# Optimization experiments

Hardware: AMD Instinct MI355X
Metric: run time of the kernel (lower is better)

## Reference

```python
import jax, jax.numpy as jnp
import numpy as np


def setup_inputs() -> dict:
    key = jax.random.key(0)
    k1, k2, k3 = jax.random.split(key, 3)
    B, S, E = 4, 8192, 1024
    x = jax.random.normal(k1, (B, S, E), dtype=jnp.float32)
    # torch nn.Linear weights have shape [out_features, in_features]
    W1 = jax.random.normal(k2, (3 * E, E), dtype=jnp.float32) * (1.0 / np.sqrt(E))
    W2 = jax.random.normal(k3, (E, E), dtype=jnp.float32) * (1.0 / np.sqrt(E))
    return {"x": x, "W1": W1, "W2": W2, "heads": 16}


def reference(x, W1, W2, heads):
    B, S, E = x.shape
    h = heads
    e = E // h
    # qkv projection: [B,S,3E] -> 'b s (n h e) -> n b h s e'
    qkv = (x @ W1.T).reshape(B, S, 3, h, e)
    qkv = jnp.transpose(qkv, (2, 0, 3, 1, 4))  # [3,B,h,S,e]
    q, k, v = qkv[0], qkv[1], qkv[2]
    # score: [B,h,e,e], softmax over last dim (c)
    score = jax.nn.softmax(jnp.einsum('bhnk,bhnc->bhkc', k / 4, v), axis=-1)
    # einsum 'bhnk,bhkc->bhnk': elementwise over k, sum over c
    attn = jax.nn.softmax(jnp.einsum('bhnk,bhkc->bhnk', q / 4, score), axis=-1)
    # 'b h s e -> b s (h e)' then linear_2
    out = jnp.transpose(attn, (0, 2, 1, 3)).reshape(B, S, E) @ W2.T
    return out
```

## Files before the change

kernel.cpp:

```cpp
#include <hip/hip_runtime.h>
#include <hip/hip_bf16.h>
#include <stdint.h>

static constexpr int MTOT = 32768;
static constexpr int KD   = 1024;
static constexpr int ND   = 1024;

static constexpr int BM = 256, BN = 256, BK = 64;
static constexpr int NT = KD / BK;
static constexpr int BUF_BYTES = 65536;
static constexpr int BOFF = 32768;
static constexpr int HALF = 16384;

typedef __bf16 bf16x8 __attribute__((ext_vector_type(8)));
typedef float  f32x4  __attribute__((ext_vector_type(4)));

__device__ __forceinline__ unsigned short f2bf_rne(float f) {
  union { float f; uint32_t u; } c; c.f = f;
  uint32_t u = c.u;
  return (unsigned short)((u + 0x7fffu + ((u >> 16) & 1u)) >> 16);
}

__global__ void cast_f32_to_bf16(const float* __restrict__ src,
                                 unsigned short* __restrict__ dst, int n4) {
  int idx = blockIdx.x * blockDim.x + threadIdx.x;
  int stride = gridDim.x * blockDim.x;
  for (int i = idx; i < n4; i += stride) {
    float4 v = reinterpret_cast<const float4*>(src)[i];
    ushort4 o;
    o.x = f2bf_rne(v.x); o.y = f2bf_rne(v.y);
    o.z = f2bf_rne(v.z); o.w = f2bf_rne(v.w);
    reinterpret_cast<ushort4*>(dst)[i] = o;
  }
}

__device__ __forceinline__ void gload_lds16(const void* g, void* lds) {
  __builtin_amdgcn_global_load_lds(
      (const __attribute__((address_space(1))) unsigned int*)g,
      (__attribute__((address_space(3))) unsigned int*)lds, 16, 0, 0);
}

template <int SOFTMAX>
__global__ __launch_bounds__(512, 2)
void gemm8(const unsigned short* __restrict__ A,
           const unsigned short* __restrict__ Bm,
           void* __restrict__ Cout) {
  extern __shared__ __align__(16) char ldsc[];

  const int tid  = threadIdx.x;
  const int lane = tid & 63;
  const int wid  = tid >> 6;
  const int wm = wid >> 2, wn = wid & 3;
  const int fr = lane & 15, fq = lane >> 4;
  const int bid  = blockIdx.x;
  const int brow = (bid >> 2) * BM;
  const int bcol = (bid & 3) * BN;

  const int srow  = tid >> 3;
  const int sslot = (tid & 7) ^ (srow & 7);
  const unsigned short* gA = A  + (size_t)(brow + srow) * KD + sslot * 8;
  const unsigned short* gB = Bm + (size_t)(bcol + srow) * KD + sslot * 8;
  const int wofs = wid << 10;

  f32x4  acc[8][4] = {};
  bf16x8 a0[4][2], a1[4][2], bb[2][2];

  auto STAGE = [&](const unsigned short* g, int h, int kt, int b, int opOff) {
    const unsigned short* gu = g + (size_t)(h * 128) * KD + kt * BK;
    char* du = ldsc + b * BUF_BYTES + opOff + h * HALF + wofs;
    gload_lds16(gu, du);
    gload_lds16(gu + (size_t)64 * KD, du + 8192);
  };

  auto rdA = [&](int b, bf16x8 (*dst)[2], int mBase) {
    const char* base = ldsc + b * BUF_BYTES + wm * HALF;
    #pragma unroll
    for (int mm = 0; mm < 4; ++mm) {
      const int r = (mBase + mm) * 16 + fr;
      #pragma unroll
      for (int ks = 0; ks < 2; ++ks)
        dst[mm][ks] = *(const bf16x8*)(base + (r << 7) +
                        ((ks * 64 + fq * 16) ^ ((r & 7) << 4)));
    }
  };
  auto rdB = [&](int b, int nBase) {
    const char* base = ldsc + b * BUF_BYTES + BOFF + (wn >> 1) * HALF;
    #pragma unroll
    for (int nn = 0; nn < 2; ++nn) {
      const int r = (wn & 1) * 64 + (nBase + nn) * 16 + fr;
      #pragma unroll
      for (int ks = 0; ks < 2; ++ks)
        bb[nn][ks] = *(const bf16x8*)(base + (r << 7) +
                       ((ks * 64 + fq * 16) ^ ((r & 7) << 4)));
    }
  };
  auto MFMA16 = [&](int mBase, int nBase, bf16x8 (*af)[2]) {
    #pragma unroll
    for (int mm = 0; mm < 4; ++mm)
      #pragma unroll
      for (int nn = 0; nn < 2; ++nn)
        #pragma unroll
        for (int ks = 0; ks < 2; ++ks)
          acc[mBase + mm][nBase + nn] = __builtin_amdgcn_mfma_f32_16x16x32_bf16(
              af[mm][ks], bb[nn][ks], acc[mBase + mm][nBase + nn], 0, 0, 0);
  };

  STAGE(gA, 0, 0, 0, 0);    STAGE(gA, 1, 0, 0, 0);
  STAGE(gB, 0, 0, 0, BOFF); STAGE(gB, 1, 0, 0, BOFF);
  STAGE(gA, 0, 1, 1, 0);    STAGE(gA, 1, 1, 1, 0);
  asm volatile("s_waitcnt vmcnt(4)" ::: "memory");
  __builtin_amdgcn_s_barrier();

  for (int T = 0; T < NT; ++T) {
    const int cur = T & 1, nxt = cur ^ 1;
    const int tp1 = (T + 1 < NT) ? T + 1 : NT - 1;
    const int tp2 = (T + 2 < NT) ? T + 2 : NT - 1;

    rdA(cur, a0, 0); rdB(cur, 0);
    STAGE(gB, 0, tp1, nxt, BOFF);
    __builtin_amdgcn_s_barrier();
    asm volatile("s_waitcnt lgkmcnt(0)" ::: "memory");
    __builtin_amdgcn_s_setprio(1);
    MFMA16(0, 0, a0);
    __builtin_amdgcn_s_setprio(0);
    __builtin_amdgcn_s_barrier();

    rdA(cur, a1, 4);
    STAGE(gB, 1, tp1, nxt, BOFF);
    __builtin_amdgcn_s_barrier();
    asm volatile("s_waitcnt lgkmcnt(0)" ::: "memory");
    __builtin_amdgcn_s_setprio(1);
    MFMA16(4, 0, a1);
    __builtin_amdgcn_s_setprio(0);
    __builtin_amdgcn_s_barrier();

    rdB(cur, 2);
    STAGE(gA, 0, tp2, cur, 0);
    __builtin_amdgcn_s_barrier();
    asm volatile("s_waitcnt lgkmcnt(0)" ::: "memory");
    __builtin_amdgcn_s_setprio(1);
    MFMA16(4, 2, a1);
    __builtin_amdgcn_s_setprio(0);
    __builtin_amdgcn_s_barrier();

    STAGE(gA, 1, tp2, cur, 0);
    asm volatile("s_waitcnt vmcnt(4)" ::: "memory");
    __builtin_amdgcn_s_barrier();
    __builtin_amdgcn_s_setprio(1);
    MFMA16(0, 2, a0);
    __builtin_amdgcn_s_setprio(0);
    __builtin_amdgcn_s_barrier();
  }

  if constexpr (SOFTMAX) {
    unsigned short* attn = reinterpret_cast<unsigned short*>(Cout);
    constexpr float CEXP = 0.25f * 1.44269504088896340736f;
    #pragma unroll
    for (int m = 0; m < 8; ++m) {
      const int row = brow + wm * 128 + m * 16 + fq * 4;
      #pragma unroll
      for (int j = 0; j < 4; ++j) {
        float v0 = acc[m][0][j], v1 = acc[m][1][j];
        float v2 = acc[m][2][j], v3 = acc[m][3][j];
        float mx = fmaxf(fmaxf(v0, v1), fmaxf(v2, v3));
        #pragma unroll
        for (int s = 1; s < 16; s <<= 1) mx = fmaxf(mx, __shfl_xor(mx, s, 64));
        float p0 = exp2f((v0 - mx) * CEXP);
        float p1 = exp2f((v1 - mx) * CEXP);
        float p2 = exp2f((v2 - mx) * CEXP);
        float p3 = exp2f((v3 - mx) * CEXP);
        float sm = p0 + p1 + p2 + p3;
        #pragma unroll
        for (int s = 1; s < 16; s <<= 1) sm += __shfl_xor(sm, s, 64);
        const float inv = 1.0f / sm;
        unsigned short* dst =
            attn + (size_t)(row + j) * ND + (bcol + wn * 64 + fr);
        dst[0]  = f2bf_rne(p0 * inv);
        dst[16] = f2bf_rne(p1 * inv);
        dst[32] = f2bf_rne(p2 * inv);
        dst[48] = f2bf_rne(p3 * inv);
      }
    }
  } else {
    float* Cf = reinterpret_cast<float*>(Cout);
    #pragma unroll
    for (int m = 0; m < 8; ++m) {
      const int row = brow + wm * 128 + m * 16 + fq * 4;
      #pragma unroll
      for (int n = 0; n < 4; ++n) {
        const int col = bcol + wn * 64 + n * 16 + fr;
        #pragma unroll
        for (int j = 0; j < 4; ++j)
          Cf[(size_t)(row + j) * ND + col] = acc[m][n][j];
      }
    }
  }
}

extern "C" void kernel_launch(void* const* d_in, const int* in_sizes, int n_in,
                              void* d_out, int out_size, void* d_ws, size_t ws_size,
                              hipStream_t stream) {
  const float* x  = (const float*)d_in[0];
  const float* W1 = (const float*)d_in[1];
  const float* W2 = (const float*)d_in[2];
  float* out = (float*)d_out;

  char* ws = (char*)d_ws;
  unsigned short* xb   = (unsigned short*)(ws);
  unsigned short* w1b  = (unsigned short*)(ws + (size_t)67108864);
  unsigned short* w2b  = (unsigned short*)(ws + (size_t)69206016);
  unsigned short* attn = (unsigned short*)(ws + (size_t)71303168);

  hipFuncSetAttribute(reinterpret_cast<const void*>(gemm8<1>),
                      hipFuncAttributeMaxDynamicSharedMemorySize, 131072);
  hipFuncSetAttribute(reinterpret_cast<const void*>(gemm8<0>),
                      hipFuncAttributeMaxDynamicSharedMemorySize, 131072);

  cast_f32_to_bf16<<<2048, 256, 0, stream>>>(x,  xb,  MTOT * KD / 4);
  cast_f32_to_bf16<<<512,  256, 0, stream>>>(W1, w1b, KD * KD / 4);
  cast_f32_to_bf16<<<512,  256, 0, stream>>>(W2, w2b, KD * KD / 4);

  const int nblk = (MTOT / BM) * (ND / BN);
  gemm8<1><<<nblk, 512, 131072, stream>>>(xb, w1b, (void*)attn);
  gemm8<0><<<nblk, 512, 131072, stream>>>(attn, w2b, (void*)out);
}
```

Measured before the change: 205.8 us.

## Prefetch next tile's B fragments during last MFMA phase and remap block order

Splits the B fragment registers into two sets. The first B fragments of the next K tile are now read from LDS during the final MFMA phase of the current iteration, so the first phase no longer waits on that read. It also remaps block indices so that consecutive workgroups spread across row tiles in groups of eight, which changes L2 reuse of the A and B operands. The cost is more live VGPRs, which risks spilling under a launch bound of 512 threads with 2 blocks per CU.

```diff
diff --git a/kernel.cpp b/kernel.cpp
--- a/kernel.cpp
+++ b/kernel.cpp
@@ -52,7 +52,9 @@
   const int wid  = tid >> 6;
   const int wm = wid >> 2, wn = wid & 3;
   const int fr = lane & 15, fq = lane >> 4;
-  const int bid  = blockIdx.x;
+
+  const int bid0 = blockIdx.x;
+  const int bid  = ((bid0 & 7) << 6) | (bid0 >> 3);
   const int brow = (bid >> 2) * BM;
   const int bcol = (bid & 3) * BN;
 
@@ -60,14 +62,14 @@
   const int sslot = (tid & 7) ^ (srow & 7);
   const unsigned short* gA = A  + (size_t)(brow + srow) * KD + sslot * 8;
   const unsigned short* gB = Bm + (size_t)(bcol + srow) * KD + sslot * 8;
-  const int wofs = wid << 10;
+  const int wofs = tid * 16;
 
   f32x4  acc[8][4] = {};
-  bf16x8 a0[4][2], a1[4][2], bb[2][2];
+  bf16x8 a0[4][2], a1[4][2], bA[2][2], bB[2][2];
 
   auto STAGE = [&](const unsigned short* g, int h, int kt, int b, int opOff) {
     const unsigned short* gu = g + (size_t)(h * 128) * KD + kt * BK;
-    char* du = ldsc + b * BUF_BYTES + opOff + h * HALF + wofs;
+    char* du = ldsc + b * BUF_BYTES + opOff + h * HALF + (wid << 10);
     gload_lds16(gu, du);
     gload_lds16(gu + (size_t)64 * KD, du + 8192);
   };
@@ -83,18 +85,18 @@
                         ((ks * 64 + fq * 16) ^ ((r & 7) << 4)));
     }
   };
-  auto rdB = [&](int b, int nBase) {
+  auto rdB = [&](int b, int nBase, bf16x8 (*dst)[2]) {
     const char* base = ldsc + b * BUF_BYTES + BOFF + (wn >> 1) * HALF;
     #pragma unroll
     for (int nn = 0; nn < 2; ++nn) {
       const int r = (wn & 1) * 64 + (nBase + nn) * 16 + fr;
       #pragma unroll
       for (int ks = 0; ks < 2; ++ks)
-        bb[nn][ks] = *(const bf16x8*)(base + (r << 7) +
+        dst[nn][ks] = *(const bf16x8*)(base + (r << 7) +
                        ((ks * 64 + fq * 16) ^ ((r & 7) << 4)));
     }
   };
-  auto MFMA16 = [&](int mBase, int nBase, bf16x8 (*af)[2]) {
+  auto MFMA16 = [&](int mBase, int nBase, bf16x8 (*af)[2], bf16x8 (*bf)[2]) {
     #pragma unroll
     for (int mm = 0; mm < 4; ++mm)
       #pragma unroll
@@ -102,7 +104,7 @@
         #pragma unroll
         for (int ks = 0; ks < 2; ++ks)
           acc[mBase + mm][nBase + nn] = __builtin_amdgcn_mfma_f32_16x16x32_bf16(
-              af[mm][ks], bb[nn][ks], acc[mBase + mm][nBase + nn], 0, 0, 0);
+              af[mm][ks], bf[nn][ks], acc[mBase + mm][nBase + nn], 0, 0, 0);
   };
 
   STAGE(gA, 0, 0, 0, 0);    STAGE(gA, 1, 0, 0, 0);
@@ -110,18 +112,19 @@
   STAGE(gA, 0, 1, 1, 0);    STAGE(gA, 1, 1, 1, 0);
   asm volatile("s_waitcnt vmcnt(4)" ::: "memory");
   __builtin_amdgcn_s_barrier();
+  rdB(0, 0, bA);
 
   for (int T = 0; T < NT; ++T) {
     const int cur = T & 1, nxt = cur ^ 1;
     const int tp1 = (T + 1 < NT) ? T + 1 : NT - 1;
     const int tp2 = (T + 2 < NT) ? T + 2 : NT - 1;
 
-    rdA(cur, a0, 0); rdB(cur, 0);
+    rdA(cur, a0, 0);
     STAGE(gB, 0, tp1, nxt, BOFF);
     __builtin_amdgcn_s_barrier();
     asm volatile("s_waitcnt lgkmcnt(0)" ::: "memory");
     __builtin_amdgcn_s_setprio(1);
-    MFMA16(0, 0, a0);
+    MFMA16(0, 0, a0, bA);
     __builtin_amdgcn_s_setprio(0);
     __builtin_amdgcn_s_barrier();
 
@@ -130,24 +133,25 @@
     __builtin_amdgcn_s_barrier();
     asm volatile("s_waitcnt lgkmcnt(0)" ::: "memory");
     __builtin_amdgcn_s_setprio(1);
-    MFMA16(4, 0, a1);
-    __builtin_amdgcn_s_setprio(0);
-    __builtin_amdgcn_s_barrier();
-
-    rdB(cur, 2);
+    MFMA16(4, 0, a1, bA);
+    __builtin_amdgcn_s_setprio(0);
+    __builtin_amdgcn_s_barrier();
+
+    rdB(cur, 2, bB);
     STAGE(gA, 0, tp2, cur, 0);
     __builtin_amdgcn_s_barrier();
     asm volatile("s_waitcnt lgkmcnt(0)" ::: "memory");
     __builtin_amdgcn_s_setprio(1);
-    MFMA16(4, 2, a1);
+    MFMA16(4, 2, a1, bB);
     __builtin_amdgcn_s_setprio(0);
     __builtin_amdgcn_s_barrier();
 
     STAGE(gA, 1, tp2, cur, 0);
     asm volatile("s_waitcnt vmcnt(4)" ::: "memory");
     __builtin_amdgcn_s_barrier();
-    __builtin_amdgcn_s_setprio(1);
-    MFMA16(0, 2, a0);
+    rdB(nxt, 0, bA);
+    __builtin_amdgcn_s_setprio(1);
+    MFMA16(0, 2, a0, bB);
     __builtin_amdgcn_s_setprio(0);
     __builtin_amdgcn_s_barrier();
   }
```

Result: faster. 197.5 us (-4.1%).
